# Kernel tuning notes

Hardware: AMD Instinct MI355X
Metric: run time of the kernel (lower is better)

Reference implementation:

```python
import jax, jax.numpy as jnp
import numpy as np

EPS = 1e-5

def _layernorm(h):
    # parameter-free LayerNorm over last dim (elementwise_affine=False)
    mu = jnp.mean(h, axis=-1, keepdims=True)
    var = jnp.mean(jnp.square(h - mu), axis=-1, keepdims=True)
    return (h - mu) / jnp.sqrt(var + EPS)

def setup_inputs() -> dict:
    key = jax.random.key(0)
    k1, k2, k3, k4 = jax.random.split(key, 4)
    B, D, F_, I = 16, 37, 4096, 64
    x = jax.random.normal(k1, (B, D, F_), dtype=jnp.float32)
    s = 1.0 / np.sqrt(D)  # ~ torch Linear default init scale
    Wq = jax.random.normal(k2, (D, I), dtype=jnp.float32) * s
    Wk = jax.random.normal(k3, (D, I), dtype=jnp.float32) * s
    Wv = jax.random.normal(k4, (D, I), dtype=jnp.float32) * s
    return {"x": x, "Wq": Wq, "Wk": Wk, "Wv": Wv}

def reference(x, Wq, Wk, Wv):
    # x: [B, depth, featuresize] -> entities [B, F, depth]
    xb = jnp.transpose(x, (0, 2, 1))
    q = _layernorm(jnp.einsum('bfd,di->bfi', xb, Wq))
    k = _layernorm(jnp.einsum('bfd,di->bfi', xb, Wk))
    v = _layernorm(jnp.einsum('bfd,di->bfi', xb, Wv))
    d = q.shape[-1]
    att = jnp.einsum('bqi,bki->bqk', q, k) / jnp.sqrt(jnp.float32(d))
    # faithful to torch: softmax over dim=1 (the query axis), not the key axis
    weights = jax.nn.softmax(att, axis=-2)
    return jnp.einsum('bqk,bki->bqi', weights, v)
```

## Files before the change

kernel.cpp:

```cpp
#include <hip/hip_runtime.h>
#include <math.h>

#define B_  16
#define D_  37
#define F_  4096
#define I_  64
#define EPS 1e-5f
#define QSCALE 0.18033688011112042f
#define NQS 4

typedef unsigned short u16;
typedef __bf16 bf16x8 __attribute__((ext_vector_type(8)));
typedef __bf16 bf16x2v __attribute__((ext_vector_type(2)));
typedef float  f32x16 __attribute__((ext_vector_type(16)));
typedef float  f32x2v __attribute__((ext_vector_type(2)));
typedef unsigned int u32x4 __attribute__((ext_vector_type(4)));
typedef int i32x2 __attribute__((ext_vector_type(2)));

#define ZERO16 {0,0,0,0, 0,0,0,0, 0,0,0,0, 0,0,0,0}
#define MFMA32(a, b, c) __builtin_amdgcn_mfma_f32_32x32x16_bf16((a), (b), (c), 0, 0, 0)

#if __has_builtin(__builtin_amdgcn_exp2f)
#define EX2(x) __builtin_amdgcn_exp2f(x)
#else
#define EX2(x) exp2f(x)
#endif
#if __has_builtin(__builtin_amdgcn_rcpf)
#define RCP(x) __builtin_amdgcn_rcpf(x)
#else
#define RCP(x) (1.f / (x))
#endif

__device__ __forceinline__ u16 f2b(float f) {
  unsigned u = __builtin_bit_cast(unsigned, f);
  return (u16)((u + 0x7fffu + ((u >> 16) & 1u)) >> 16);
}
__device__ __forceinline__ float b2f(u16 h) {
  return __builtin_bit_cast(float, (unsigned)h << 16);
}
__device__ __forceinline__ unsigned pk2(float lo, float hi) {
  f32x2v f = {lo, hi};
  bf16x2v h = __builtin_convertvector(f, bf16x2v);
  return __builtin_bit_cast(unsigned, h);
}

__device__ __forceinline__ void plswap(unsigned& a, unsigned& b) {
#if __has_builtin(__builtin_amdgcn_permlane32_swap)
  i32x2 r = __builtin_amdgcn_permlane32_swap((int)a, (int)b, false, false);
  a = (unsigned)r[0];
  b = (unsigned)r[1];
#else
  const int lh = (int)((threadIdx.x & 63) >> 5);
  unsigned pa = (unsigned)__shfl_xor((int)a, 32, 64);
  unsigned pb = (unsigned)__shfl_xor((int)b, 32, 64);
  unsigned na = lh ? pb : a;
  unsigned nb = lh ? b : pa;
  a = na;
  b = nb;
#endif
}

__device__ __forceinline__ void build_af(const f32x16& s, bf16x8& f0, bf16x8& f1) {
  float e[16];
#pragma unroll
  for (int r = 0; r < 16; ++r) e[r] = EX2(s[r]);
  unsigned a = pk2(e[0], e[1]),   bq = pk2(e[2], e[3]);
  unsigned c = pk2(e[4], e[5]),   d  = pk2(e[6], e[7]);
  plswap(a, c);
  plswap(bq, d);
  u32x4 v0 = {a, bq, c, d};
  f0 = __builtin_bit_cast(bf16x8, v0);
  unsigned ee = pk2(e[8], e[9]),  ff = pk2(e[10], e[11]);
  unsigned g  = pk2(e[12], e[13]), h = pk2(e[14], e[15]);
  plswap(ee, g);
  plswap(ff, h);
  u32x4 v1 = {ee, ff, g, h};
  f1 = __builtin_bit_cast(bf16x8, v1);
}

__device__ __forceinline__ bf16x8 ldfrag(const u16* base, int row, int kb) {
  return *(const bf16x8*)(base + (row << 6) + ((kb ^ (row & 7)) << 3));
}
__device__ __forceinline__ void stage16(u16* dst, const u16* src, int c, int spitch) {
  const int r = c >> 3, cb = c & 7;
  const int4 v = *(const int4*)(src + (size_t)r * spitch + (cb << 3));
  *(int4*)(dst + (r << 6) + ((cb ^ (r & 7)) << 3)) = v;
}
__device__ __forceinline__ int soff_l(int c) {
  const int r = c >> 3, cb = c & 7;
  return (r << 6) + ((cb ^ (r & 7)) << 3);
}
__device__ __forceinline__ int soff_g(int c, int spitch) {
  return (c >> 3) * spitch + ((c & 7) << 3);
}

__global__ __launch_bounds__(256) void qkv_ln_k(
    const float* __restrict__ x,
    const float* __restrict__ Wq, const float* __restrict__ Wk,
    const float* __restrict__ Wv,
    u16* __restrict__ qn, u16* __restrict__ kn, u16* __restrict__ vt) {
  __shared__ float sW[3 * D_ * I_];
  __shared__ float xs[D_ * 64];
  __shared__ __align__(16) u16 vtile[64 * 72];

  const int t = threadIdx.x;
  const int b = blockIdx.y;
  const int f0 = blockIdx.x * 64;

  for (int i = t; i < D_ * I_; i += 256) {
    sW[i]               = Wq[i];
    sW[D_ * I_ + i]     = Wk[i];
    sW[2 * D_ * I_ + i] = Wv[i];
  }
  const float* xb = x + (size_t)b * D_ * F_ + f0;
  for (int i = t; i < D_ * 64; i += 256)
    xs[i] = xb[(size_t)(i >> 6) * F_ + (i & 63)];
  __syncthreads();

  const int lane = t & 63, w = t >> 6;

  for (int it = 0; it < 16; ++it) {
    const int fl = w * 16 + it;
    float hq = 0.f, hk = 0.f, hv = 0.f;
#pragma unroll
    for (int d = 0; d < D_; ++d) {
      const float xv = xs[d * 64 + fl];
      hq = fmaf(xv, sW[d * 64 + lane], hq);
      hk = fmaf(xv, sW[D_ * I_ + d * 64 + lane], hk);
      hv = fmaf(xv, sW[2 * D_ * I_ + d * 64 + lane], hv);
    }
    auto lnorm = [&](float a) -> float {
      float s = a;
#pragma unroll
      for (int o = 32; o > 0; o >>= 1) s += __shfl_xor(s, o, 64);
      const float mu = s * (1.f / 64.f);
      const float d0 = a - mu;
      float v = d0 * d0;
#pragma unroll
      for (int o = 32; o > 0; o >>= 1) v += __shfl_xor(v, o, 64);
      return d0 * rsqrtf(v * (1.f / 64.f) + EPS);
    };
    const size_t fo = ((size_t)b * F_ + f0 + fl) * I_ + lane;
    qn[fo] = f2b(lnorm(hq) * QSCALE);
    kn[fo] = f2b(lnorm(hk));
    vtile[lane * 72 + fl] = f2b(lnorm(hv));
  }
  __syncthreads();
  for (int p = 0; p < 2; ++p) {
    const int c = p * 256 + t;
    const int r = c >> 3, off = (c & 7) * 8;
    const int4 v = *(const int4*)&vtile[r * 72 + off];
    *(int4*)(vt + ((size_t)b * I_ + r) * F_ + f0 + off) = v;
  }
}

__global__ __launch_bounds__(256, 4) void attn_stats_k(
    const u16* __restrict__ qn, const u16* __restrict__ kn,
    float* __restrict__ zp) {
  __shared__ __align__(16) u16 sm[16384];

  const int t = threadIdx.x, lane = t & 63, w = t >> 6;
  const int l31 = lane & 31, lh = lane >> 5;
  const int b = blockIdx.y, k0 = blockIdx.x * 256, qh = blockIdx.z;

  const u16* kb = kn + ((size_t)b * F_ + k0) * I_;
#pragma unroll
  for (int p = 0; p < 8; ++p) stage16(sm, kb, p * 256 + t, 64);
  __syncthreads();
  bf16x8 kf[2][4];
#pragma unroll
  for (int kb2 = 0; kb2 < 2; ++kb2)
#pragma unroll
    for (int ic = 0; ic < 4; ++ic)
      kf[kb2][ic] = ldfrag(sm + (w * 64 + kb2 * 32) * 64, l31, ic * 2 + lh);
  __syncthreads();

  int qoff_l[2], qoff_g[2];
#pragma unroll
  for (int p = 0; p < 2; ++p) {
    const int c = p * 256 + t;
    qoff_l[p] = soff_l(c);
    qoff_g[p] = soff_g(c, 64);
  }

  const u16* qsrc = qn + ((size_t)b * F_ + qh * (F_ / NQS)) * I_;
#pragma unroll
  for (int p = 0; p < 2; ++p)
    *(int4*)(sm + qoff_l[p]) = *(const int4*)(qsrc + qoff_g[p]);
  qsrc += 64 * I_;

  float Zc[2][2] = {{0.f, 0.f}, {0.f, 0.f}};
  const int NC = F_ / NQS / 64;

  for (int c = 0; c < NC; ++c) {
    const int cur = (c & 1) * 4096;
    int4 qr0, qr1;
    const bool pf = (c + 1 < NC);
    if (pf) {
      qr0 = *(const int4*)(qsrc + qoff_g[0]);
      qr1 = *(const int4*)(qsrc + qoff_g[1]);
      qsrc += 64 * I_;
    }
    __syncthreads();

    f32x16 a00 = ZERO16, a01 = ZERO16, a10 = ZERO16, a11 = ZERO16;
    __builtin_amdgcn_s_setprio(1);
#pragma unroll
    for (int ic = 0; ic < 4; ++ic) {
      const bf16x8 q0f = ldfrag(sm + cur, l31, ic * 2 + lh);
      const bf16x8 q1f = ldfrag(sm + cur + 32 * 64, l31, ic * 2 + lh);
      a00 = MFMA32(q0f, kf[0][ic], a00);
      a01 = MFMA32(q0f, kf[1][ic], a01);
      a10 = MFMA32(q1f, kf[0][ic], a10);
      a11 = MFMA32(q1f, kf[1][ic], a11);
    }
    __builtin_amdgcn_s_setprio(0);
#pragma unroll
    for (int r = 0; r < 16; ++r) {
      Zc[0][0] += EX2(a00[r]);
      Zc[0][1] += EX2(a01[r]);
      Zc[1][0] += EX2(a10[r]);
      Zc[1][1] += EX2(a11[r]);
    }

    if (pf) {
      const int nxt = cur ^ 4096;
      *(int4*)(sm + nxt + qoff_l[0]) = qr0;
      *(int4*)(sm + nxt + qoff_l[1]) = qr1;
    }
  }

#pragma unroll
  for (int kb2 = 0; kb2 < 2; ++kb2) {
    float Zt = Zc[0][kb2] + Zc[1][kb2];
    Zt += __shfl_xor(Zt, 32, 64);
    if (lane < 32)
      zp[((size_t)qh * B_ + b) * F_ + k0 + w * 64 + kb2 * 32 + lane] = Zt;
  }
}

__global__ __launch_bounds__(256) void vscale_k(u16* __restrict__ vt,
                                                const float* __restrict__ zp) {
  const int b = blockIdx.y;
  const int off = (blockIdx.x * 256 + (int)threadIdx.x) * 8;
  const int k = off & (F_ - 1);
  const size_t BF = (size_t)B_ * F_;
  u16* p = vt + (size_t)b * I_ * F_ + off;
  const float* z = zp + (size_t)b * F_ + k;
  int4 raw = *(const int4*)p;
  u16 es[8], os[8];
  *(int4*)es = raw;
#pragma unroll
  for (int j = 0; j < 8; ++j) {
    const float v = b2f(es[j]);
    float zs = 0.f;
#pragma unroll
    for (int qh = 0; qh < NQS; ++qh) zs += z[qh * BF + j];
    os[j] = f2b(v * RCP(zs));
  }
  *(int4*)p = *(int4*)os;
}

__global__ __launch_bounds__(256, 4) void attn_out_k(
    const u16* __restrict__ qn, const u16* __restrict__ kn,
    const u16* __restrict__ vt, float* __restrict__ out,
    u16* __restrict__ pout) {
  __shared__ __align__(16) u16 sm[16384];

  const int t = threadIdx.x, lane = t & 63, w = t >> 6;
  const int l31 = lane & 31, lh = lane >> 5;
  const int b = blockIdx.y, q0 = blockIdx.x * 128, ks = blockIdx.z;

  const u16* qb = qn + ((size_t)b * F_ + q0) * I_;
#pragma unroll
  for (int p = 0; p < 4; ++p) stage16(sm, qb, p * 256 + t, 64);
  __syncthreads();
  bf16x8 qf[4];
#pragma unroll
  for (int ic = 0; ic < 4; ++ic)
    qf[ic] = ldfrag(sm + (w * 32) * 64, l31, ic * 2 + lh);
  __syncthreads();

  int off_l[2], kg[2], vg[2];
#pragma unroll
  for (int p = 0; p < 2; ++p) {
    const int c = p * 256 + t;
    off_l[p] = soff_l(c);
    kg[p] = soff_g(c, 64);
    vg[p] = soff_g(c, F_);
  }

  const u16* ksrc = kn + ((size_t)b * F_ + ks * (F_ / 2)) * I_;
  const u16* vsrc = vt + (size_t)b * I_ * F_ + ks * (F_ / 2);
#pragma unroll
  for (int p = 0; p < 2; ++p) {
    *(int4*)(sm + off_l[p])        = *(const int4*)(ksrc + kg[p]);
    *(int4*)(sm + 8192 + off_l[p]) = *(const int4*)(vsrc + vg[p]);
  }
  ksrc += 64 * I_;
  vsrc += 64;

  f32x16 o0 = ZERO16, o1 = ZERO16;
  const int NC = F_ / 2 / 64;

  for (int c = 0; c < NC; ++c) {
    const int cur = (c & 1) * 4096;
    int4 kr0, kr1, vr0, vr1;
    const bool pf = (c + 1 < NC);
    if (pf) {
      kr0 = *(const int4*)(ksrc + kg[0]);
      kr1 = *(const int4*)(ksrc + kg[1]);
      vr0 = *(const int4*)(vsrc + vg[0]);
      vr1 = *(const int4*)(vsrc + vg[1]);
      ksrc += 64 * I_;
      vsrc += 64;
    }
    __syncthreads();

    const u16* Kc = sm + cur;
    f32x16 s0 = ZERO16, s1 = ZERO16;
    __builtin_amdgcn_s_setprio(1);
#pragma unroll
    for (int ic = 0; ic < 4; ++ic) {
      const bf16x8 ak0 = ldfrag(Kc, l31, ic * 2 + lh);
      const bf16x8 ak1 = ldfrag(Kc + 32 * 64, l31, ic * 2 + lh);
      s0 = MFMA32(ak0, qf[ic], s0);
      s1 = MFMA32(ak1, qf[ic], s1);
    }
    __builtin_amdgcn_s_setprio(0);

    bf16x8 af[4];
    build_af(s0, af[0], af[1]);
    build_af(s1, af[2], af[3]);

    const u16* Vc = sm + 8192 + cur;
    __builtin_amdgcn_s_setprio(1);
#pragma unroll
    for (int kb4 = 0; kb4 < 4; ++kb4) {
      const bf16x8 bv0 = ldfrag(Vc, l31, kb4 * 2 + lh);
      const bf16x8 bv1 = ldfrag(Vc + 32 * 64, l31, kb4 * 2 + lh);
      o0 = MFMA32(af[kb4], bv0, o0);
      o1 = MFMA32(af[kb4], bv1, o1);
    }
    __builtin_amdgcn_s_setprio(0);

    if (pf) {
      const int nxt = cur ^ 4096;
      *(int4*)(sm + nxt + off_l[0])        = kr0;
      *(int4*)(sm + nxt + off_l[1])        = kr1;
      *(int4*)(sm + 8192 + nxt + off_l[0]) = vr0;
      *(int4*)(sm + 8192 + nxt + off_l[1]) = vr1;
    }
  }

  if (ks == 0) {
    float* ob = out + ((size_t)b * F_ + q0 + w * 32) * I_;
#pragma unroll
    for (int r = 0; r < 16; ++r) {
      const int qr = (r & 3) + 8 * (r >> 2) + 4 * lh;
      ob[(size_t)qr * I_ + l31]      = o0[r];
      ob[(size_t)qr * I_ + 32 + l31] = o1[r];
    }
  } else {
    u16* pb = pout + ((size_t)b * F_ + q0 + w * 32) * I_;
#pragma unroll
    for (int r = 0; r < 16; ++r) {
      const int qr = (r & 3) + 8 * (r >> 2) + 4 * lh;
      pb[(size_t)qr * I_ + l31]      = f2b(o0[r]);
      pb[(size_t)qr * I_ + 32 + l31] = f2b(o1[r]);
    }
  }
}

__global__ __launch_bounds__(256) void reduce_k(float* __restrict__ out,
                                                const u16* __restrict__ pout) {
  const size_t i = ((size_t)blockIdx.x * 256 + threadIdx.x) * 8;
  float4 a0 = *(const float4*)(out + i);
  float4 a1 = *(const float4*)(out + i + 4);
  int4 praw = *(const int4*)(pout + i);
  u16 es[8];
  *(int4*)es = praw;
  a0.x += b2f(es[0]); a0.y += b2f(es[1]); a0.z += b2f(es[2]); a0.w += b2f(es[3]);
  a1.x += b2f(es[4]); a1.y += b2f(es[5]); a1.z += b2f(es[6]); a1.w += b2f(es[7]);
  *(float4*)(out + i)     = a0;
  *(float4*)(out + i + 4) = a1;
}

extern "C" void kernel_launch(void* const* d_in, const int* in_sizes, int n_in,
                              void* d_out, int out_size, void* d_ws,
                              size_t ws_size, hipStream_t stream) {
  const float* x  = (const float*)d_in[0];
  const float* Wq = (const float*)d_in[1];
  const float* Wk = (const float*)d_in[2];
  const float* Wv = (const float*)d_in[3];
  float* out = (float*)d_out;

  const size_t NBF = (size_t)B_ * F_ * I_;
  u16* qn   = (u16*)d_ws;
  u16* kn   = qn + NBF;
  u16* vt   = kn + NBF;
  float* zp = (float*)(vt + NBF);
  u16* pout = (u16*)(zp + (size_t)NQS * B_ * F_);

  qkv_ln_k<<<dim3(F_ / 64, B_), 256, 0, stream>>>(x, Wq, Wk, Wv, qn, kn, vt);
  attn_stats_k<<<dim3(F_ / 256, B_, NQS), 256, 0, stream>>>(qn, kn, zp);
  vscale_k<<<dim3(I_ * F_ / 2048, B_), 256, 0, stream>>>(vt, zp);
  attn_out_k<<<dim3(F_ / 128, B_, 2), 256, 0, stream>>>(qn, kn, vt, out, pout);
  reduce_k<<<dim3((int)(NBF / 2048)), 256, 0, stream>>>(out, pout);
}
```

Baseline: 244.0 us.

## Double query tile per block, halve stats split, swizzle grid for XCD locality

attn_out_k now handles 256 queries per block (64 per wave) with four accumulator tiles, so each staged K/V chunk is reused across twice as many queries. attn_stats_k drops from 4 to 2 query splits. Both kernels use a flat 512-block grid with a swizzle that sends blocks of the same batch to the same XCD, aiming for better L2 reuse. Launch bounds fall to 2 blocks per SM to make room for the extra registers, which lowers occupancy and leaves about 2 blocks per CU.

```diff
diff --git a/kernel.cpp b/kernel.cpp
--- a/kernel.cpp
+++ b/kernel.cpp
@@ -7,7 +7,7 @@
 #define I_  64
 #define EPS 1e-5f
 #define QSCALE 0.18033688011112042f
-#define NQS 4
+#define NQS 2
 
 typedef unsigned short u16;
 typedef __bf16 bf16x8 __attribute__((ext_vector_type(8)));
@@ -94,6 +94,10 @@
   return (c >> 3) * spitch + ((c & 7) << 3);
 }
 
+__device__ __forceinline__ int swz512(int wg) {
+  return (wg & 7) * 64 + (wg >> 3);
+}
+
 __global__ __launch_bounds__(256) void qkv_ln_k(
     const float* __restrict__ x,
     const float* __restrict__ Wq, const float* __restrict__ Wk,
@@ -154,14 +158,15 @@
   }
 }
 
-__global__ __launch_bounds__(256, 4) void attn_stats_k(
+__global__ __launch_bounds__(256, 2) void attn_stats_k(
     const u16* __restrict__ qn, const u16* __restrict__ kn,
     float* __restrict__ zp) {
   __shared__ __align__(16) u16 sm[16384];
 
   const int t = threadIdx.x, lane = t & 63, w = t >> 6;
   const int l31 = lane & 31, lh = lane >> 5;
-  const int b = blockIdx.y, k0 = blockIdx.x * 256, qh = blockIdx.z;
+  const int lg = swz512((int)blockIdx.x);
+  const int k0 = (lg & 15) * 256, b = (lg >> 4) & 15, qh = lg >> 8;
 
   const u16* kb = kn + ((size_t)b * F_ + k0) * I_;
 #pragma unroll
@@ -261,7 +266,7 @@
   *(int4*)p = *(int4*)os;
 }
 
-__global__ __launch_bounds__(256, 4) void attn_out_k(
+__global__ __launch_bounds__(256, 2) void attn_out_k(
     const u16* __restrict__ qn, const u16* __restrict__ kn,
     const u16* __restrict__ vt, float* __restrict__ out,
     u16* __restrict__ pout) {
@@ -269,16 +274,19 @@
 
   const int t = threadIdx.x, lane = t & 63, w = t >> 6;
   const int l31 = lane & 31, lh = lane >> 5;
-  const int b = blockIdx.y, q0 = blockIdx.x * 128, ks = blockIdx.z;
+  const int lg = swz512((int)blockIdx.x);
+  const int q0 = (lg & 15) * 256, b = (lg >> 4) & 15, ks = lg >> 8;
 
   const u16* qb = qn + ((size_t)b * F_ + q0) * I_;
 #pragma unroll
-  for (int p = 0; p < 4; ++p) stage16(sm, qb, p * 256 + t, 64);
-  __syncthreads();
-  bf16x8 qf[4];
-#pragma unroll
-  for (int ic = 0; ic < 4; ++ic)
-    qf[ic] = ldfrag(sm + (w * 32) * 64, l31, ic * 2 + lh);
+  for (int p = 0; p < 8; ++p) stage16(sm, qb, p * 256 + t, 64);
+  __syncthreads();
+  bf16x8 qf[2][4];
+#pragma unroll
+  for (int qb2 = 0; qb2 < 2; ++qb2)
+#pragma unroll
+    for (int ic = 0; ic < 4; ++ic)
+      qf[qb2][ic] = ldfrag(sm + (w * 64 + qb2 * 32) * 64, l31, ic * 2 + lh);
   __syncthreads();
 
   int off_l[2], kg[2], vg[2];
@@ -300,7 +308,7 @@
   ksrc += 64 * I_;
   vsrc += 64;
 
-  f32x16 o0 = ZERO16, o1 = ZERO16;
+  f32x16 o00 = ZERO16, o01 = ZERO16, o10 = ZERO16, o11 = ZERO16;
   const int NC = F_ / 2 / 64;
 
   for (int c = 0; c < NC; ++c) {
@@ -318,20 +326,24 @@
     __syncthreads();
 
     const u16* Kc = sm + cur;
-    f32x16 s0 = ZERO16, s1 = ZERO16;
+    f32x16 s00 = ZERO16, s01 = ZERO16, s10 = ZERO16, s11 = ZERO16;
     __builtin_amdgcn_s_setprio(1);
 #pragma unroll
     for (int ic = 0; ic < 4; ++ic) {
       const bf16x8 ak0 = ldfrag(Kc, l31, ic * 2 + lh);
       const bf16x8 ak1 = ldfrag(Kc + 32 * 64, l31, ic * 2 + lh);
-      s0 = MFMA32(ak0, qf[ic], s0);
-      s1 = MFMA32(ak1, qf[ic], s1);
+      s00 = MFMA32(ak0, qf[0][ic], s00);
+      s01 = MFMA32(ak0, qf[1][ic], s01);
+      s10 = MFMA32(ak1, qf[0][ic], s10);
+      s11 = MFMA32(ak1, qf[1][ic], s11);
     }
     __builtin_amdgcn_s_setprio(0);
 
-    bf16x8 af[4];
-    build_af(s0, af[0], af[1]);
-    build_af(s1, af[2], af[3]);
+    bf16x8 af[2][4];
+    build_af(s00, af[0][0], af[0][1]);
+    build_af(s10, af[0][2], af[0][3]);
+    build_af(s01, af[1][0], af[1][1]);
+    build_af(s11, af[1][2], af[1][3]);
 
     const u16* Vc = sm + 8192 + cur;
     __builtin_amdgcn_s_setprio(1);
@@ -339,8 +351,10 @@
     for (int kb4 = 0; kb4 < 4; ++kb4) {
       const bf16x8 bv0 = ldfrag(Vc, l31, kb4 * 2 + lh);
       const bf16x8 bv1 = ldfrag(Vc + 32 * 64, l31, kb4 * 2 + lh);
-      o0 = MFMA32(af[kb4], bv0, o0);
-      o1 = MFMA32(af[kb4], bv1, o1);
+      o00 = MFMA32(af[0][kb4], bv0, o00);
+      o01 = MFMA32(af[0][kb4], bv1, o01);
+      o10 = MFMA32(af[1][kb4], bv0, o10);
+      o11 = MFMA32(af[1][kb4], bv1, o11);
     }
     __builtin_amdgcn_s_setprio(0);
 
@@ -354,20 +368,24 @@
   }
 
   if (ks == 0) {
-    float* ob = out + ((size_t)b * F_ + q0 + w * 32) * I_;
+    float* ob = out + ((size_t)b * F_ + q0 + w * 64) * I_;
 #pragma unroll
     for (int r = 0; r < 16; ++r) {
       const int qr = (r & 3) + 8 * (r >> 2) + 4 * lh;
-      ob[(size_t)qr * I_ + l31]      = o0[r];
-      ob[(size_t)qr * I_ + 32 + l31] = o1[r];
+      ob[(size_t)qr * I_ + l31]              = o00[r];
+      ob[(size_t)qr * I_ + 32 + l31]         = o01[r];
+      ob[(size_t)(32 + qr) * I_ + l31]       = o10[r];
+      ob[(size_t)(32 + qr) * I_ + 32 + l31]  = o11[r];
     }
   } else {
-    u16* pb = pout + ((size_t)b * F_ + q0 + w * 32) * I_;
+    u16* pb = pout + ((size_t)b * F_ + q0 + w * 64) * I_;
 #pragma unroll
     for (int r = 0; r < 16; ++r) {
       const int qr = (r & 3) + 8 * (r >> 2) + 4 * lh;
-      pb[(size_t)qr * I_ + l31]      = f2b(o0[r]);
-      pb[(size_t)qr * I_ + 32 + l31] = f2b(o1[r]);
+      pb[(size_t)qr * I_ + l31]              = f2b(o00[r]);
+      pb[(size_t)qr * I_ + 32 + l31]         = f2b(o01[r]);
+      pb[(size_t)(32 + qr) * I_ + l31]       = f2b(o10[r]);
+      pb[(size_t)(32 + qr) * I_ + 32 + l31]  = f2b(o11[r]);
     }
   }
 }
@@ -403,8 +421,8 @@
   u16* pout = (u16*)(zp + (size_t)NQS * B_ * F_);
 
   qkv_ln_k<<<dim3(F_ / 64, B_), 256, 0, stream>>>(x, Wq, Wk, Wv, qn, kn, vt);
-  attn_stats_k<<<dim3(F_ / 256, B_, NQS), 256, 0, stream>>>(qn, kn, zp);
+  attn_stats_k<<<dim3(512), 256, 0, stream>>>(qn, kn, zp);
   vscale_k<<<dim3(I_ * F_ / 2048, B_), 256, 0, stream>>>(vt, zp);
-  attn_out_k<<<dim3(F_ / 128, B_, 2), 256, 0, stream>>>(qn, kn, vt, out, pout);
+  attn_out_k<<<dim3(512), 256, 0, stream>>>(qn, kn, vt, out, pout);
   reduce_k<<<dim3((int)(NBF / 2048)), 256, 0, stream>>>(out, pout);
 }
```

Result: faster. 234.6 us (-3.8%).
